# Kernel optimization log

Hardware: AMD Instinct MI355X
Metric: run time of the kernel (lower is better)

Reference implementation:

```python
import jax, jax.numpy as jnp
import numpy as np

D = 256  # input_dim


def setup_inputs() -> dict:
    key = jax.random.key(0)
    ks = jax.random.split(key, 10)
    s = 1.0 / np.sqrt(D)  # torch Linear init scale (uniform bound)
    desc0 = jax.random.normal(ks[0], (4, 4096, D), dtype=jnp.float32)
    desc1 = jax.random.normal(ks[1], (4, 4096, D), dtype=jnp.float32)
    def lin(kw, kb):
        W = jax.random.uniform(kw, (D, D), jnp.float32, -s, s)
        b = jax.random.uniform(kb, (D,), jnp.float32, -s, s)
        return W, b
    Wq, bq = lin(ks[2], ks[3])
    Wk, bk = lin(ks[4], ks[5])
    Wv, bv = lin(ks[6], ks[7])
    Wo, bo = lin(ks[8], ks[9])
    return {"desc0": desc0, "desc1": desc1,
            "Wq": Wq, "bq": bq, "Wk": Wk, "bk": bk,
            "Wv": Wv, "bv": bv, "Wo": Wo, "bo": bo}


def reference(desc0, desc1, Wq, bq, Wk, bk, Wv, bv, Wo, bo):
    # torch Linear: y = x @ W.T + b
    q = desc0 @ Wq.T + bq                      # [B, N0, D]
    k = desc1 @ Wk.T + bk                      # [B, N1, D]
    v = desc1 @ Wv.T + bv                      # [B, N1, D]
    scale = 1.0 / jnp.sqrt(jnp.asarray(q.shape[-1], q.dtype))
    attn = jnp.einsum('bqd,bkd->bqk', q, k) * scale  # [B, N0, N1]
    weights = jax.nn.softmax(attn, axis=-1)
    out = jnp.einsum('bqk,bkd->bqd', weights, v)     # [B, N0, D]
    return out @ Wo.T + bo
```

## Files before the change

### kernel.cpp

```cpp
#include <hip/hip_runtime.h>


typedef __attribute__((ext_vector_type(8))) __bf16 bf16x8;
typedef __attribute__((ext_vector_type(4))) float f32x4;
typedef __attribute__((ext_vector_type(16))) float f32x16;
typedef __attribute__((ext_vector_type(4))) unsigned int u32x4;
typedef __attribute__((ext_vector_type(2))) unsigned int u32x2;
typedef __attribute__((ext_vector_type(4))) unsigned short us16x4;

__device__ __forceinline__ unsigned short f2bf(float f) {
  unsigned u = __builtin_bit_cast(unsigned, f);
  u += 0x7FFFu + ((u >> 16) & 1u);
  return (unsigned short)(u >> 16);
}
__device__ __forceinline__ unsigned pk2(float a, float b) {
  return (unsigned)f2bf(a) | ((unsigned)f2bf(b) << 16);
}
__device__ __forceinline__ unsigned cvtpk(float lo, float hi) {
  unsigned r;
  asm("v_cvt_pk_bf16_f32 %0, %1, %2" : "=v"(r) : "v"(lo), "v"(hi));
  return r;
}
__device__ __forceinline__ float bf2f(unsigned short s) {
  return __builtin_bit_cast(float, ((unsigned)s) << 16);
}
__device__ __forceinline__ int swz4(int r) { return (r ^ (r >> 2)) & 3; }
__device__ __forceinline__ bf16x8 ldbf16(const void* p) {
  return __builtin_bit_cast(bf16x8, *(const u32x4*)p);
}
__device__ __forceinline__ f32x4 mfma16(bf16x8 a, bf16x8 b, f32x4 c) {
  return __builtin_amdgcn_mfma_f32_16x16x32_bf16(a, b, c, 0, 0, 0);
}
__device__ __forceinline__ f32x16 mfma32(bf16x8 a, bf16x8 b, f32x16 c) {
  return __builtin_amdgcn_mfma_f32_32x32x16_bf16(a, b, c, 0, 0, 0);
}
__device__ __forceinline__ void gld16(void* lds, const void* gsrc) {
  __builtin_amdgcn_global_load_lds(
      (const __attribute__((address_space(1))) unsigned int*)gsrc,
      (__attribute__((address_space(3))) unsigned int*)lds, 16, 0, 0);
}

template <int IN_BF16, int MODE>
__global__ __launch_bounds__(256, 4) void proj_k(const void* __restrict__ Ain,
                                                 const float* __restrict__ W,
                                                 const float* __restrict__ bias,
                                                 void* __restrict__ Cout) {
  __shared__ __align__(16) unsigned short Al[2][64 * 32];
  __shared__ __align__(16) unsigned short Wl[2][64 * 32];
  __shared__ float biasl[64];
  const int tid = threadIdx.x;
  const int w = tid >> 6, l = tid & 63, g = l >> 4, c = l & 15;
  const int mt = blockIdx.x & 255, nq = blockIdx.x >> 8;
  const int row0 = mt * 64, n0 = nq * 64;
  if (tid < 64) biasl[tid] = bias[n0 + tid];

  const int sr = tid >> 2, seg = tid & 3;
  const int ssw = swz4(sr);

  {
    if (IN_BF16) {
      const unsigned short* ap = (const unsigned short*)Ain + (size_t)(row0 + sr) * 256 + seg * 8;
      *(u32x4*)&Al[0][sr * 32 + ((seg ^ ssw) << 3)] = *(const u32x4*)ap;
    } else {
      const float* ap = (const float*)Ain + (size_t)(row0 + sr) * 256 + seg * 8;
      float4 x = *(const float4*)ap, y = *(const float4*)(ap + 4);
      u32x4 v; v[0] = pk2(x.x, x.y); v[1] = pk2(x.z, x.w); v[2] = pk2(y.x, y.y); v[3] = pk2(y.z, y.w);
      *(u32x4*)&Al[0][sr * 32 + ((seg ^ ssw) << 3)] = v;
    }
    const float* wp = W + (size_t)(n0 + sr) * 256 + seg * 8;
    float4 x = *(const float4*)wp, y = *(const float4*)(wp + 4);
    u32x4 v; v[0] = pk2(x.x, x.y); v[1] = pk2(x.z, x.w); v[2] = pk2(y.x, y.y); v[3] = pk2(y.z, y.w);
    *(u32x4*)&Wl[0][sr * 32 + ((seg ^ ssw) << 3)] = v;
  }
  __syncthreads();

  f32x4 acc[4];
#pragma unroll
  for (int jt = 0; jt < 4; ++jt) acc[jt] = (f32x4){0.f, 0.f, 0.f, 0.f};

#pragma unroll 1
  for (int ch = 0; ch < 8; ++ch) {
    const int cur = ch & 1;
    const bool pre = (ch + 1 < 8);
    float4 ax, ay, wx, wy; u32x4 abv;
    if (pre) {
      const int ko = (ch + 1) * 32 + seg * 8;
      if (IN_BF16) {
        abv = *(const u32x4*)((const unsigned short*)Ain + (size_t)(row0 + sr) * 256 + ko);
      } else {
        const float* ap = (const float*)Ain + (size_t)(row0 + sr) * 256 + ko;
        ax = *(const float4*)ap; ay = *(const float4*)(ap + 4);
      }
      const float* wp = W + (size_t)(n0 + sr) * 256 + ko;
      wx = *(const float4*)wp; wy = *(const float4*)(wp + 4);
    }
    const int ra = w * 16 + c;
    bf16x8 af = ldbf16(&Al[cur][ra * 32 + ((g ^ swz4(ra)) << 3)]);
#pragma unroll
    for (int jt = 0; jt < 4; ++jt) {
      const int j = jt * 16 + c;
      bf16x8 bfr = ldbf16(&Wl[cur][j * 32 + ((g ^ swz4(j)) << 3)]);
      acc[jt] = mfma16(af, bfr, acc[jt]);
    }
    if (pre) {
      u32x4 v;
      if (IN_BF16) v = abv;
      else { v[0] = pk2(ax.x, ax.y); v[1] = pk2(ax.z, ax.w); v[2] = pk2(ay.x, ay.y); v[3] = pk2(ay.z, ay.w); }
      *(u32x4*)&Al[1 - cur][sr * 32 + ((seg ^ ssw) << 3)] = v;
      u32x4 vw; vw[0] = pk2(wx.x, wx.y); vw[1] = pk2(wx.z, wx.w); vw[2] = pk2(wy.x, wy.y); vw[3] = pk2(wy.z, wy.w);
      *(u32x4*)&Wl[1 - cur][sr * 32 + ((seg ^ ssw) << 3)] = vw;
    }
    __syncthreads();
  }

#pragma unroll
  for (int jt = 0; jt < 4; ++jt) {
    const int col = n0 + jt * 16 + c;
    const float bv = biasl[jt * 16 + c];
    const int rloc = w * 16 + (g << 2);
    if (MODE == 0) {
      unsigned short* q = (unsigned short*)Cout;
#pragma unroll
      for (int r = 0; r < 4; ++r)
        q[(size_t)(row0 + rloc + r) * 256 + col] = f2bf(acc[jt][r] + bv);
    } else if (MODE == 1) {
      unsigned short* vt = (unsigned short*)Cout;
      const int n = row0 + rloc;
      const int b = n >> 12, nl = n & 4095;
      us16x4 pk;
      pk[0] = f2bf(acc[jt][0] + bv); pk[1] = f2bf(acc[jt][1] + bv);
      pk[2] = f2bf(acc[jt][2] + bv); pk[3] = f2bf(acc[jt][3] + bv);
      *(us16x4*)(vt + (size_t)b * 1048576 + (size_t)(nl >> 6) * 16384 + col * 64 + (nl & 63)) = pk;
    } else if (MODE == 2) {
      float* o = (float*)Cout;
#pragma unroll
      for (int r = 0; r < 4; ++r)
        o[(size_t)(row0 + rloc + r) * 256 + col] = acc[jt][r] + bv;
    } else {
      unsigned short* kq = (unsigned short*)Cout;
      const int kst = (n0 >> 4) + jt;
      const int j = c & 7, hb = c >> 3;
#pragma unroll
      for (int r = 0; r < 4; ++r) {
        const int n = row0 + rloc + r;
        kq[(size_t)(n >> 5) * 8192 + kst * 512 + (((n & 31) + hb * 32) << 3) + j] =
            f2bf(acc[jt][r] + bv);
      }
    }
  }
}

template <int NS>
__global__ __launch_bounds__(512, 2) void attn_k(const unsigned short* __restrict__ qg,
                                                 const unsigned short* __restrict__ kfb,
                                                 const unsigned short* __restrict__ vg,
                                                 unsigned short* __restrict__ part,
                                                 float* __restrict__ lw) {
  __shared__ __align__(16) unsigned char smem[132096];
  const int tid = threadIdx.x, w = tid >> 6, l = tid & 63;
  const int l31 = l & 31, h5 = l >> 5;
  const int qt = w >> 1, hf = w & 1;
  const int bid = blockIdx.x;
  const int b4 = bid & 3;
  const int s = (NS == 2) ? ((bid >> 2) & 1) : 0;
  const int qtl = (NS == 2) ? (bid >> 3) : (bid >> 2);
  const int q0 = qtl * 128;
  const int NT = (NS == 2) ? 32 : 64;

  const unsigned short* kb = kfb + (size_t)b4 * 1048576 + (size_t)s * 524288;
  const unsigned short* vb = vg + (size_t)b4 * 1048576 + (size_t)s * 32 * 16384;

  bf16x8 qf[16];
  {
    const unsigned short* qp = qg + ((size_t)b4 * 4096 + q0 + qt * 32 + l31) * 256;
#pragma unroll
    for (int kst = 0; kst < 16; ++kst) qf[kst] = ldbf16(qp + kst * 16 + h5 * 8);
  }

  f32x16 o[4];
#pragma unroll
  for (int d = 0; d < 4; ++d)
#pragma unroll
    for (int r = 0; r < 16; ++r) o[d][r] = 0.f;
  float l_run = 0.f;

  int goffV[4];
#pragma unroll
  for (int i = 0; i < 4; ++i) {
    const int sl = i * 512 + tid;
    const int r = sl >> 4, p16 = sl & 15;
    const int x = p16 ^ (r & 15);
    goffV[i] = (2 * r + (x >> 3)) * 64 + ((x & 7) << 3);
  }
#define STAGEV(buf, t1)                                                            \
  {                                                                                \
    const unsigned short* _vs = vb + (size_t)(t1) * 16384;                         \
    _Pragma("unroll") for (int i = 0; i < 4; ++i)                                  \
        gld16(smem + (buf) * 32768 + i * 8192 + w * 1024, _vs + goffV[i]);         \
  }
#define LOADK(dst, t1)                                                             \
  {                                                                                \
    const unsigned short* _tb = kb + (size_t)((t1) * 2 + hf) * 8192 + l * 8;       \
    _Pragma("unroll") for (int kst = 0; kst < 16; ++kst)                           \
        dst[kst] = *(const u32x4*)(_tb + kst * 512);                               \
  }

  u32x4 kf[16];
  LOADK(kf, 0);
  STAGEV(0, 0);
  __syncthreads();

  const float alpha = 0.09016844f;
  unsigned char* Pq = smem + 65536 + qt * 4096;

#pragma unroll 1
  for (int t = 0; t < NT; ++t) {
    const int cur = t & 1;
    if (t + 1 < NT) STAGEV(1 - cur, t + 1);

    f32x16 sa, sb;
#pragma unroll
    for (int r = 0; r < 16; ++r) { sa[r] = 0.f; sb[r] = 0.f; }
    __builtin_amdgcn_s_setprio(1);
#pragma unroll
    for (int kst = 0; kst < 16; ++kst) {
      bf16x8 kfr = __builtin_bit_cast(bf16x8, kf[kst]);
      if (kst & 1) sb = mfma32(kfr, qf[kst], sb);
      else         sa = mfma32(kfr, qf[kst], sa);
    }
    __builtin_amdgcn_s_setprio(0);

    float p[16];
#pragma unroll
    for (int r = 0; r < 16; ++r) p[r] = exp2f((sa[r] + sb[r]) * alpha);
    float ls = ((p[0] + p[1]) + (p[2] + p[3])) + ((p[4] + p[5]) + (p[6] + p[7])) +
               (((p[8] + p[9]) + (p[10] + p[11])) + ((p[12] + p[13]) + (p[14] + p[15])));
    ls += __shfl_xor(ls, 32);
    l_run += ls;

    unsigned u[8];
#pragma unroll
    for (int i = 0; i < 8; ++i) u[i] = cvtpk(p[2 * i], p[2 * i + 1]);
#pragma unroll
    for (int j = 0; j < 4; ++j) {
      u32x2 dv; dv[0] = u[2 * j]; dv[1] = u[2 * j + 1];
      *(u32x2*)(Pq + l31 * 128 + (((j + 4 * hf) ^ (l31 & 7)) << 4) + h5 * 8) = dv;
    }

    if (t + 1 < NT) LOADK(kf, t + 1);

    asm volatile("s_waitcnt lgkmcnt(0)\n\ts_barrier" ::: "memory");
    __builtin_amdgcn_sched_barrier(0);

    bf16x8 pb[4];
#pragma unroll
    for (int kst = 0; kst < 4; ++kst)
      pb[kst] = ldbf16(Pq + l31 * 128 + (((kst * 2 + h5) ^ (l31 & 7)) << 4));
    const unsigned char* Vc = smem + cur * 32768;
    __builtin_amdgcn_s_setprio(1);
#pragma unroll
    for (int dsub = 0; dsub < 4; ++dsub) {
      const int dm = hf * 128 + dsub * 32 + l31;
      const int r = dm >> 1;
      const unsigned char* Vr = Vc + r * 256;
      const int xb = (dm & 1) * 8;
#pragma unroll
      for (int kst = 0; kst < 4; ++kst) {
        bf16x8 vf = ldbf16(Vr + (((xb + kst * 2 + h5) ^ (r & 15)) << 4));
        o[dsub] = mfma32(vf, pb[kst], o[dsub]);
      }
    }
    __builtin_amdgcn_s_setprio(0);

    __syncthreads();
  }
#undef STAGEV
#undef LOADK

  float* Lb = (float*)(smem + 131072);
  if (l < 32) Lb[(qt * 2 + hf) * 32 + l31] = l_run;
  __syncthreads();

  unsigned char* T = smem + w * 16384;
#pragma unroll
  for (int dsub = 0; dsub < 4; ++dsub)
#pragma unroll
    for (int rg = 0; rg < 4; ++rg) {
      f32x4 wv;
      wv[0] = o[dsub][4 * rg + 0]; wv[1] = o[dsub][4 * rg + 1];
      wv[2] = o[dsub][4 * rg + 2]; wv[3] = o[dsub][4 * rg + 3];
      const int d4 = dsub * 8 + rg * 2 + h5;
      *(f32x4*)(T + l31 * 512 + ((d4 ^ l31) << 4)) = wv;
    }
  asm volatile("s_waitcnt lgkmcnt(0)" ::: "memory");
  __builtin_amdgcn_sched_barrier(0);
  {
    const int q2 = l >> 1, dh = l & 1;
    unsigned short* op = part + (size_t)s * 4194304 +
                         ((size_t)b4 * 4096 + q0 + qt * 32 + q2) * 256 + hf * 128 + dh * 64;
#pragma unroll
    for (int jj = 0; jj < 8; ++jj) {
      f32x4 r0 = *(const f32x4*)(T + q2 * 512 + (((dh * 16 + 2 * jj) ^ q2) << 4));
      f32x4 r1 = *(const f32x4*)(T + q2 * 512 + (((dh * 16 + 2 * jj + 1) ^ q2) << 4));
      u32x4 ov;
      ov[0] = pk2(r0[0], r0[1]); ov[1] = pk2(r0[2], r0[3]);
      ov[2] = pk2(r1[0], r1[1]); ov[3] = pk2(r1[2], r1[3]);
      *(u32x4*)(op + jj * 8) = ov;
    }
  }
  if (hf == 0 && l < 32) {
    const float lt = Lb[(qt * 2) * 32 + l31] + Lb[(qt * 2 + 1) * 32 + l31];
    lw[(size_t)s * 16384 + (size_t)b4 * 4096 + q0 + qt * 32 + l31] = lt;
  }
}

__global__ __launch_bounds__(256, 8) void merge_k(unsigned short* __restrict__ part,
                                                  const float* __restrict__ lw, int ns) {
  const int idx = blockIdx.x * 256 + threadIdx.x;
  const int q = idx >> 5, d8 = (idx & 31) * 8;
  unsigned short* p0 = part + (size_t)q * 256 + d8;
  u32x4 a = *(const u32x4*)p0;
  float acc[8];
#pragma unroll
  for (int i = 0; i < 4; ++i) {
    acc[2 * i] = bf2f((unsigned short)(a[i] & 0xFFFF));
    acc[2 * i + 1] = bf2f((unsigned short)(a[i] >> 16));
  }
  float lt = lw[q];
  if (ns == 2) {
    u32x4 b = *(const u32x4*)(p0 + 4194304);
#pragma unroll
    for (int i = 0; i < 4; ++i) {
      acc[2 * i] += bf2f((unsigned short)(b[i] & 0xFFFF));
      acc[2 * i + 1] += bf2f((unsigned short)(b[i] >> 16));
    }
    lt += lw[16384 + q];
  }
  const float inv = 1.f / lt;
  u32x4 ov;
#pragma unroll
  for (int i = 0; i < 4; ++i) ov[i] = pk2(acc[2 * i] * inv, acc[2 * i + 1] * inv);
  *(u32x4*)p0 = ov;
}

extern "C" void kernel_launch(void* const* d_in, const int* in_sizes, int n_in,
                              void* d_out, int out_size, void* d_ws, size_t ws_size,
                              hipStream_t stream) {
  (void)in_sizes; (void)n_in; (void)out_size;
  const float* desc0 = (const float*)d_in[0];
  const float* desc1 = (const float*)d_in[1];
  const float* Wq = (const float*)d_in[2];
  const float* bq = (const float*)d_in[3];
  const float* Wk = (const float*)d_in[4];
  const float* bk = (const float*)d_in[5];
  const float* Wv = (const float*)d_in[6];
  const float* bv = (const float*)d_in[7];
  const float* Wo = (const float*)d_in[8];
  const float* bo = (const float*)d_in[9];

  unsigned char* ws = (unsigned char*)d_ws;
  unsigned short* qw = (unsigned short*)(ws);
  unsigned short* kw = (unsigned short*)(ws + 8388608);
  unsigned short* vw = (unsigned short*)(ws + 16777216);
  unsigned short* part = (unsigned short*)(ws + 25165824);
  float* lwp = (float*)(ws + 41943040);

  const bool two = (ws_size >= 42008576ull);

  proj_k<0, 0><<<1024, 256, 0, stream>>>(desc0, Wq, bq, qw);
  proj_k<0, 3><<<1024, 256, 0, stream>>>(desc1, Wk, bk, kw);
  proj_k<0, 1><<<1024, 256, 0, stream>>>(desc1, Wv, bv, vw);
  if (two) {
    attn_k<2><<<256, 512, 0, stream>>>(qw, kw, vw, part, lwp);
    merge_k<<<2048, 256, 0, stream>>>(part, lwp, 2);
  } else {
    lwp = (float*)(ws + 33554432);
    attn_k<1><<<128, 512, 0, stream>>>(qw, kw, vw, part, lwp);
    merge_k<<<2048, 256, 0, stream>>>(part, lwp, 1);
  }
  proj_k<1, 2><<<1024, 256, 0, stream>>>(part, Wo, bo, (float*)d_out);
}
```

Measured before the change: 141.1 us.

## Fuse split-merge into output projection and software-pipeline PV behind QK

The separate merge kernel is removed. Its job of summing the two split partials and dividing by the softmax denominator now happens inside the output projection's A-tile load. The attention loop is also restructured: V moves to a triple buffer and P to a double buffer, so the PV product of the previous tile runs after the QK of the current tile. This removes the mid-iteration barrier, and the K fragment load is moved earlier. The price is more LDS, extra live registers, and an epilogue PV step; removing the merge kernel also saves a launch and a global read/write pass.

```diff
diff --git a/kernel.cpp b/kernel.cpp
--- a/kernel.cpp
+++ b/kernel.cpp
@@ -40,11 +40,12 @@
       (__attribute__((address_space(3))) unsigned int*)lds, 16, 0, 0);
 }
 
-template <int IN_BF16, int MODE>
+template <int IN_MODE, int MODE>
 __global__ __launch_bounds__(256, 4) void proj_k(const void* __restrict__ Ain,
                                                  const float* __restrict__ W,
                                                  const float* __restrict__ bias,
-                                                 void* __restrict__ Cout) {
+                                                 void* __restrict__ Cout,
+                                                 const float* __restrict__ lwA) {
   __shared__ __align__(16) unsigned short Al[2][64 * 32];
   __shared__ __align__(16) unsigned short Wl[2][64 * 32];
   __shared__ float biasl[64];
@@ -57,10 +58,33 @@
   const int sr = tid >> 2, seg = tid & 3;
   const int ssw = swz4(sr);
 
+  float ainv = 1.f;
+  if (IN_MODE >= 2) {
+    const int grow = row0 + sr;
+    float lt = lwA[grow];
+    if (IN_MODE == 2) lt += lwA[16384 + grow];
+    ainv = 1.f / lt;
+  }
+
   {
-    if (IN_BF16) {
+    if (IN_MODE == 1) {
       const unsigned short* ap = (const unsigned short*)Ain + (size_t)(row0 + sr) * 256 + seg * 8;
       *(u32x4*)&Al[0][sr * 32 + ((seg ^ ssw) << 3)] = *(const u32x4*)ap;
+    } else if (IN_MODE >= 2) {
+      const unsigned short* ap = (const unsigned short*)Ain + (size_t)(row0 + sr) * 256 + seg * 8;
+      u32x4 a0 = *(const u32x4*)ap, v;
+      u32x4 a1 = (IN_MODE == 2) ? *(const u32x4*)(ap + 4194304) : a0;
+#pragma unroll
+      for (int i = 0; i < 4; ++i) {
+        float lo = bf2f((unsigned short)(a0[i] & 0xFFFF));
+        float hi = bf2f((unsigned short)(a0[i] >> 16));
+        if (IN_MODE == 2) {
+          lo += bf2f((unsigned short)(a1[i] & 0xFFFF));
+          hi += bf2f((unsigned short)(a1[i] >> 16));
+        }
+        v[i] = pk2(lo * ainv, hi * ainv);
+      }
+      *(u32x4*)&Al[0][sr * 32 + ((seg ^ ssw) << 3)] = v;
     } else {
       const float* ap = (const float*)Ain + (size_t)(row0 + sr) * 256 + seg * 8;
       float4 x = *(const float4*)ap, y = *(const float4*)(ap + 4);
@@ -82,11 +106,15 @@
   for (int ch = 0; ch < 8; ++ch) {
     const int cur = ch & 1;
     const bool pre = (ch + 1 < 8);
-    float4 ax, ay, wx, wy; u32x4 abv;
+    float4 ax, ay, wx, wy; u32x4 abv, abv2;
     if (pre) {
       const int ko = (ch + 1) * 32 + seg * 8;
-      if (IN_BF16) {
+      if (IN_MODE == 1) {
         abv = *(const u32x4*)((const unsigned short*)Ain + (size_t)(row0 + sr) * 256 + ko);
+      } else if (IN_MODE >= 2) {
+        const unsigned short* ap = (const unsigned short*)Ain + (size_t)(row0 + sr) * 256 + ko;
+        abv = *(const u32x4*)ap;
+        if (IN_MODE == 2) abv2 = *(const u32x4*)(ap + 4194304);
       } else {
         const float* ap = (const float*)Ain + (size_t)(row0 + sr) * 256 + ko;
         ax = *(const float4*)ap; ay = *(const float4*)(ap + 4);
@@ -104,8 +132,21 @@
     }
     if (pre) {
       u32x4 v;
-      if (IN_BF16) v = abv;
-      else { v[0] = pk2(ax.x, ax.y); v[1] = pk2(ax.z, ax.w); v[2] = pk2(ay.x, ay.y); v[3] = pk2(ay.z, ay.w); }
+      if (IN_MODE == 1) v = abv;
+      else if (IN_MODE >= 2) {
+#pragma unroll
+        for (int i = 0; i < 4; ++i) {
+          float lo = bf2f((unsigned short)(abv[i] & 0xFFFF));
+          float hi = bf2f((unsigned short)(abv[i] >> 16));
+          if (IN_MODE == 2) {
+            lo += bf2f((unsigned short)(abv2[i] & 0xFFFF));
+            hi += bf2f((unsigned short)(abv2[i] >> 16));
+          }
+          v[i] = pk2(lo * ainv, hi * ainv);
+        }
+      } else {
+        v[0] = pk2(ax.x, ax.y); v[1] = pk2(ax.z, ax.w); v[2] = pk2(ay.x, ay.y); v[3] = pk2(ay.z, ay.w);
+      }
       *(u32x4*)&Al[1 - cur][sr * 32 + ((seg ^ ssw) << 3)] = v;
       u32x4 vw; vw[0] = pk2(wx.x, wx.y); vw[1] = pk2(wx.z, wx.w); vw[2] = pk2(wy.x, wy.y); vw[3] = pk2(wy.z, wy.w);
       *(u32x4*)&Wl[1 - cur][sr * 32 + ((seg ^ ssw) << 3)] = vw;
@@ -204,6 +245,26 @@
     _Pragma("unroll") for (int kst = 0; kst < 16; ++kst)                           \
         dst[kst] = *(const u32x4*)(_tb + kst * 512);                               \
   }
+#define PVBODY(pbuf, vbuf)                                                         \
+  {                                                                                \
+    const unsigned char* Pr = smem + 98304 + (pbuf) * 16384 + qt * 4096;           \
+    bf16x8 pb[4];                                                                  \
+    _Pragma("unroll") for (int kst = 0; kst < 4; ++kst)                            \
+        pb[kst] = ldbf16(Pr + l31 * 128 + (((kst * 2 + h5) ^ (l31 & 7)) << 4));    \
+    const unsigned char* Vc = smem + (vbuf) * 32768;                               \
+    __builtin_amdgcn_s_setprio(1);                                                 \
+    _Pragma("unroll") for (int dsub = 0; dsub < 4; ++dsub) {                       \
+      const int dm = hf * 128 + dsub * 32 + l31;                                   \
+      const int rr = dm >> 1;                                                      \
+      const unsigned char* Vr = Vc + rr * 256;                                     \
+      const int xb = (dm & 1) * 8;                                                 \
+      _Pragma("unroll") for (int kst = 0; kst < 4; ++kst) {                        \
+        bf16x8 vf = ldbf16(Vr + (((xb + kst * 2 + h5) ^ (rr & 15)) << 4));         \
+        o[dsub] = mfma32(vf, pb[kst], o[dsub]);                                    \
+      }                                                                            \
+    }                                                                              \
+    __builtin_amdgcn_s_setprio(0);                                                 \
+  }
 
   u32x4 kf[16];
   LOADK(kf, 0);
@@ -211,12 +272,14 @@
   __syncthreads();
 
   const float alpha = 0.09016844f;
-  unsigned char* Pq = smem + 65536 + qt * 4096;
+  int vst = 1, vpv = 0;
 
 #pragma unroll 1
   for (int t = 0; t < NT; ++t) {
-    const int cur = t & 1;
-    if (t + 1 < NT) STAGEV(1 - cur, t + 1);
+    if (t + 1 < NT) {
+      STAGEV(vst, t + 1);
+      vst = (vst == 2) ? 0 : vst + 1;
+    }
 
     f32x16 sa, sb;
 #pragma unroll
@@ -229,6 +292,8 @@
       else         sa = mfma32(kfr, qf[kst], sa);
     }
     __builtin_amdgcn_s_setprio(0);
+
+    if (t + 1 < NT) LOADK(kf, t + 1);
 
     float p[16];
 #pragma unroll
@@ -241,41 +306,24 @@
     unsigned u[8];
 #pragma unroll
     for (int i = 0; i < 8; ++i) u[i] = cvtpk(p[2 * i], p[2 * i + 1]);
+    unsigned char* Pq = smem + 98304 + (t & 1) * 16384 + qt * 4096;
 #pragma unroll
     for (int j = 0; j < 4; ++j) {
       u32x2 dv; dv[0] = u[2 * j]; dv[1] = u[2 * j + 1];
       *(u32x2*)(Pq + l31 * 128 + (((j + 4 * hf) ^ (l31 & 7)) << 4) + h5 * 8) = dv;
     }
 
-    if (t + 1 < NT) LOADK(kf, t + 1);
-
-    asm volatile("s_waitcnt lgkmcnt(0)\n\ts_barrier" ::: "memory");
-    __builtin_amdgcn_sched_barrier(0);
-
-    bf16x8 pb[4];
-#pragma unroll
-    for (int kst = 0; kst < 4; ++kst)
-      pb[kst] = ldbf16(Pq + l31 * 128 + (((kst * 2 + h5) ^ (l31 & 7)) << 4));
-    const unsigned char* Vc = smem + cur * 32768;
-    __builtin_amdgcn_s_setprio(1);
-#pragma unroll
-    for (int dsub = 0; dsub < 4; ++dsub) {
-      const int dm = hf * 128 + dsub * 32 + l31;
-      const int r = dm >> 1;
-      const unsigned char* Vr = Vc + r * 256;
-      const int xb = (dm & 1) * 8;
-#pragma unroll
-      for (int kst = 0; kst < 4; ++kst) {
-        bf16x8 vf = ldbf16(Vr + (((xb + kst * 2 + h5) ^ (r & 15)) << 4));
-        o[dsub] = mfma32(vf, pb[kst], o[dsub]);
-      }
-    }
-    __builtin_amdgcn_s_setprio(0);
+    if (t > 0) {
+      PVBODY((t - 1) & 1, vpv);
+      vpv = (vpv == 2) ? 0 : vpv + 1;
+    }
 
     __syncthreads();
   }
+  PVBODY((NT - 1) & 1, (NT - 1) % 3);
 #undef STAGEV
 #undef LOADK
+#undef PVBODY
 
   float* Lb = (float*)(smem + 131072);
   if (l < 32) Lb[(qt * 2 + hf) * 32 + l31] = l_run;
@@ -312,35 +360,6 @@
     const float lt = Lb[(qt * 2) * 32 + l31] + Lb[(qt * 2 + 1) * 32 + l31];
     lw[(size_t)s * 16384 + (size_t)b4 * 4096 + q0 + qt * 32 + l31] = lt;
   }
-}
-
-__global__ __launch_bounds__(256, 8) void merge_k(unsigned short* __restrict__ part,
-                                                  const float* __restrict__ lw, int ns) {
-  const int idx = blockIdx.x * 256 + threadIdx.x;
-  const int q = idx >> 5, d8 = (idx & 31) * 8;
-  unsigned short* p0 = part + (size_t)q * 256 + d8;
-  u32x4 a = *(const u32x4*)p0;
-  float acc[8];
-#pragma unroll
-  for (int i = 0; i < 4; ++i) {
-    acc[2 * i] = bf2f((unsigned short)(a[i] & 0xFFFF));
-    acc[2 * i + 1] = bf2f((unsigned short)(a[i] >> 16));
-  }
-  float lt = lw[q];
-  if (ns == 2) {
-    u32x4 b = *(const u32x4*)(p0 + 4194304);
-#pragma unroll
-    for (int i = 0; i < 4; ++i) {
-      acc[2 * i] += bf2f((unsigned short)(b[i] & 0xFFFF));
-      acc[2 * i + 1] += bf2f((unsigned short)(b[i] >> 16));
-    }
-    lt += lw[16384 + q];
-  }
-  const float inv = 1.f / lt;
-  u32x4 ov;
-#pragma unroll
-  for (int i = 0; i < 4; ++i) ov[i] = pk2(acc[2 * i] * inv, acc[2 * i + 1] * inv);
-  *(u32x4*)p0 = ov;
 }
 
 extern "C" void kernel_launch(void* const* d_in, const int* in_sizes, int n_in,
@@ -367,16 +386,15 @@
 
   const bool two = (ws_size >= 42008576ull);
 
-  proj_k<0, 0><<<1024, 256, 0, stream>>>(desc0, Wq, bq, qw);
-  proj_k<0, 3><<<1024, 256, 0, stream>>>(desc1, Wk, bk, kw);
-  proj_k<0, 1><<<1024, 256, 0, stream>>>(desc1, Wv, bv, vw);
+  proj_k<0, 0><<<1024, 256, 0, stream>>>(desc0, Wq, bq, qw, nullptr);
+  proj_k<0, 3><<<1024, 256, 0, stream>>>(desc1, Wk, bk, kw, nullptr);
+  proj_k<0, 1><<<1024, 256, 0, stream>>>(desc1, Wv, bv, vw, nullptr);
   if (two) {
     attn_k<2><<<256, 512, 0, stream>>>(qw, kw, vw, part, lwp);
-    merge_k<<<2048, 256, 0, stream>>>(part, lwp, 2);
+    proj_k<2, 2><<<1024, 256, 0, stream>>>(part, Wo, bo, (float*)d_out, lwp);
   } else {
     lwp = (float*)(ws + 33554432);
     attn_k<1><<<128, 512, 0, stream>>>(qw, kw, vw, part, lwp);
-    merge_k<<<2048, 256, 0, stream>>>(part, lwp, 1);
-  }
-  proj_k<1, 2><<<1024, 256, 0, stream>>>(part, Wo, bo, (float*)d_out);
-}
+    proj_k<3, 2><<<1024, 256, 0, stream>>>(part, Wo, bo, (float*)d_out, lwp);
+  }
+}
```

New measurement: 147.7 us. 4.7% more time.
